# Kernel tuning notes

Hardware: AMD Instinct MI355X
Metric: run time of the kernel (lower is better)

## Reference

```python
import jax, jax.numpy as jnp
import numpy as np

P = 64  # number of parameters per grid cell
# torch.combinations(param, 2, with_replacement=True) enumerates (i,j) with i<=j
# in row-major order, which matches np.triu_indices.
IDX_I, IDX_J = np.triu_indices(P)  # each length C = P*(P+1)//2 = 2080


def setup_inputs() -> dict:
    key = jax.random.key(0)
    k1, k2 = jax.random.split(key)
    # [B, G1, G2, P]
    param_tensor = jax.random.normal(k1, (32, 64, 64, P), dtype=jnp.float32)
    # [G1, G2, C]
    coeffs = jax.random.normal(k2, (64, 64, len(IDX_I)), dtype=jnp.float32)
    return {"param_tensor": param_tensor, "coeffs": coeffs}


def reference(param_tensor, coeffs):
    # Pairwise products with replacement: p_i * p_j for i <= j  -> [B,G1,G2,C]
    pair = param_tensor[..., IDX_I] * param_tensor[..., IDX_J]
    # Per-cell weighted sum over combinations, then sum over the 2D grid -> [B]
    cell = jnp.einsum('bijc,ijc->bij', pair, coeffs)
    return cell.sum(axis=(1, 2))
```

## Files before the change

kernel.cpp:

```cpp
#include <hip/hip_runtime.h>

#define NP     64
#define NC     2080
#define NCELLS 4096
#define NB     32
#define CELLS_PER_BLOCK 4
#define BLOCKS (NCELLS / CELLS_PER_BLOCK)

typedef short bf16x8 __attribute__((ext_vector_type(8)));
typedef float f32x16 __attribute__((ext_vector_type(16)));

__device__ __forceinline__ short f2bf(float f) {
  unsigned u = __float_as_uint(f);
  u += 0x7fffu + ((u >> 16) & 1u);
  return (short)(u >> 16);
}

__global__ __launch_bounds__(256, 4) void poly_mfma_kernel(
    const float* __restrict__ param,
    const float* __restrict__ coeffs,
    float* __restrict__ ws) {
  __shared__ float scoef[CELLS_PER_BLOCK][NC];
  __shared__ float sred[CELLS_PER_BLOCK][NB];

  const int tid  = threadIdx.x;
  const int wave = tid >> 6;
  const int lane = tid & 63;
  const int lo5  = lane & 31;
  const int hi   = lane >> 5;
  const int cell = blockIdx.x * CELLS_PER_BLOCK + wave;

  {
    const float4* gsrc =
        reinterpret_cast<const float4*>(coeffs + (size_t)cell * NC);
    float4* ldst = reinterpret_cast<float4*>(&scoef[wave][0]);
#pragma unroll
    for (int k = 0; k < 8; ++k) ldst[k * 64 + lane] = gsrc[k * 64 + lane];
    if (lane < 8) ldst[512 + lane] = gsrc[512 + lane];
  }

  const float* pb = param + ((size_t)lo5 * NCELLS + cell) * NP;
  bf16x8 afrag[4];
#pragma unroll
  for (int ks = 0; ks < 4; ++ks) {
#pragma unroll
    for (int eh = 0; eh < 2; ++eh) {
      const int i0 = ks * 16 + 4 * hi + 8 * eh;
      const float4 v = *reinterpret_cast<const float4*>(pb + i0);
      afrag[ks][eh * 4 + 0] = f2bf(v.x);
      afrag[ks][eh * 4 + 1] = f2bf(v.y);
      afrag[ks][eh * 4 + 2] = f2bf(v.z);
      afrag[ks][eh * 4 + 3] = f2bf(v.w);
    }
  }

  const float* sw = &scoef[wave][0];
  f32x16 acc0, acc1;
#pragma unroll
  for (int r = 0; r < 16; ++r) { acc0[r] = 0.f; acc1[r] = 0.f; }

#pragma unroll
  for (int ks = 0; ks < 4; ++ks) {
    bf16x8 b0, b1;
#pragma unroll
    for (int e = 0; e < 8; ++e) {
      const int i = ks * 16 + 4 * hi + (e & 3) + 8 * (e >> 2);
      const int cbase = i * (127 - i) / 2;
      const float v0 = (lo5 >= i) ? sw[cbase + lo5] : 0.f;
      const float v1 = (lo5 + 32 >= i) ? sw[cbase + lo5 + 32] : 0.f;
      b0[e] = f2bf(v0);
      b1[e] = f2bf(v1);
    }
    acc0 = __builtin_amdgcn_mfma_f32_32x32x16_bf16(afrag[ks], b0, acc0, 0, 0, 0);
    acc1 = __builtin_amdgcn_mfma_f32_32x32x16_bf16(afrag[ks], b1, acc1, 0, 0, 0);
  }

  float dacc[16];
#pragma unroll
  for (int r = 0; r < 16; ++r) {
    const int b = (r & 3) + 8 * (r >> 2) + 4 * hi;
    const float* pe = param + ((size_t)b * NCELLS + cell) * NP;
    dacc[r] = fmaf(acc0[r], pe[lo5], acc1[r] * pe[lo5 + 32]);
  }

#pragma unroll
  for (int r = 0; r < 16; ++r) {
    float v = dacc[r];
    v += __shfl_xor(v, 1, 64);
    v += __shfl_xor(v, 2, 64);
    v += __shfl_xor(v, 4, 64);
    v += __shfl_xor(v, 8, 64);
    v += __shfl_xor(v, 16, 64);
    dacc[r] = v;
  }
  if (lo5 == 0) {
#pragma unroll
    for (int r = 0; r < 16; ++r) {
      const int b = (r & 3) + 8 * (r >> 2) + 4 * hi;
      sred[wave][b] = dacc[r];
    }
  }
  __syncthreads();
  if (tid < NB) {
    ws[(size_t)blockIdx.x * NB + tid] =
        sred[0][tid] + sred[1][tid] + sred[2][tid] + sred[3][tid];
  }
}

__global__ void poly_reduce_kernel(const float* __restrict__ ws,
                                   float* __restrict__ out) {
  __shared__ float sred[8][NB];
  const int tid = threadIdx.x;
  const int b = tid & 31;
  const int part = tid >> 5;
  float s = 0.f;
  for (int k = 0; k < BLOCKS / 8; ++k) {
    s += ws[(size_t)(part * (BLOCKS / 8) + k) * NB + b];
  }
  sred[part][b] = s;
  __syncthreads();
  if (tid < NB) {
    float t = 0.f;
#pragma unroll
    for (int q = 0; q < 8; ++q) t += sred[q][tid];
    out[tid] = t;
  }
}

extern "C" void kernel_launch(void* const* d_in, const int* in_sizes, int n_in,
                              void* d_out, int out_size, void* d_ws,
                              size_t ws_size, hipStream_t stream) {
  const float* param = (const float*)d_in[0];
  const float* coeffs = (const float*)d_in[1];
  float* out = (float*)d_out;
  float* ws = (float*)d_ws;

  hipLaunchKernelGGL(poly_mfma_kernel, dim3(BLOCKS), dim3(256), 0, stream,
                     param, coeffs, ws);
  hipLaunchKernelGGL(poly_reduce_kernel, dim3(1), dim3(256), 0, stream, ws,
                     out);
}
```

Measured before the change: 24.26 us.

## Store coefficients as bf16 in LDS, prefetch epilogue params, parallelize final reduction

Coefficients are now converted to bf16 once during a block-cooperative load into a half-sized padded LDS buffer, so the MFMA loop reads shorts instead of converting floats each time. The epilogue parameter loads are issued before the MFMA loop to hide their latency. The workspace is transposed so the final reduction runs as 32 blocks, one per batch element, each doing a vectorized load and a shuffle reduction instead of a single block looping serially. A block-wide barrier is added after the LDS fill, and the prefetched values raise register pressure.

```diff
diff --git a/kernel.cpp b/kernel.cpp
--- a/kernel.cpp
+++ b/kernel.cpp
@@ -6,9 +6,11 @@
 #define NB     32
 #define CELLS_PER_BLOCK 4
 #define BLOCKS (NCELLS / CELLS_PER_BLOCK)
+#define CSTRIDE 2112
 
-typedef short bf16x8 __attribute__((ext_vector_type(8)));
-typedef float f32x16 __attribute__((ext_vector_type(16)));
+typedef short bf16x8  __attribute__((ext_vector_type(8)));
+typedef short short4v __attribute__((ext_vector_type(4)));
+typedef float f32x16  __attribute__((ext_vector_type(16)));
 
 __device__ __forceinline__ short f2bf(float f) {
   unsigned u = __float_as_uint(f);
@@ -20,7 +22,7 @@
     const float* __restrict__ param,
     const float* __restrict__ coeffs,
     float* __restrict__ ws) {
-  __shared__ float scoef[CELLS_PER_BLOCK][NC];
+  __shared__ short scoefh[CELLS_PER_BLOCK][CSTRIDE];
   __shared__ float sred[CELLS_PER_BLOCK][NB];
 
   const int tid  = threadIdx.x;
@@ -28,15 +30,25 @@
   const int lane = tid & 63;
   const int lo5  = lane & 31;
   const int hi   = lane >> 5;
-  const int cell = blockIdx.x * CELLS_PER_BLOCK + wave;
+  const int cellbase = blockIdx.x * CELLS_PER_BLOCK;
+  const int cell = cellbase + wave;
 
   {
     const float4* gsrc =
-        reinterpret_cast<const float4*>(coeffs + (size_t)cell * NC);
-    float4* ldst = reinterpret_cast<float4*>(&scoef[wave][0]);
+        reinterpret_cast<const float4*>(coeffs + (size_t)cellbase * NC);
 #pragma unroll
-    for (int k = 0; k < 8; ++k) ldst[k * 64 + lane] = gsrc[k * 64 + lane];
-    if (lane < 8) ldst[512 + lane] = gsrc[512 + lane];
+    for (int k = 0; k < 9; ++k) {
+      const int idx = tid + k * 256;
+      if (idx < (CELLS_PER_BLOCK * NC) / 4) {
+        const int cl = idx / 520;
+        const int q  = idx - cl * 520;
+        const float4 v = gsrc[idx];
+        short4v h;
+        h[0] = f2bf(v.x); h[1] = f2bf(v.y);
+        h[2] = f2bf(v.z); h[3] = f2bf(v.w);
+        *reinterpret_cast<short4v*>(&scoefh[cl][4 * q]) = h;
+      }
+    }
   }
 
   const float* pb = param + ((size_t)lo5 * NCELLS + cell) * NP;
@@ -54,7 +66,18 @@
     }
   }
 
-  const float* sw = &scoef[wave][0];
+  __syncthreads();
+
+  float pepi0[16], pepi1[16];
+#pragma unroll
+  for (int r = 0; r < 16; ++r) {
+    const int b = (r & 3) + 8 * (r >> 2) + 4 * hi;
+    const float* pe = param + ((size_t)b * NCELLS + cell) * NP;
+    pepi0[r] = pe[lo5];
+    pepi1[r] = pe[lo5 + 32];
+  }
+
+  const short* sw = &scoefh[wave][0];
   f32x16 acc0, acc1;
 #pragma unroll
   for (int r = 0; r < 16; ++r) { acc0[r] = 0.f; acc1[r] = 0.f; }
@@ -66,10 +89,10 @@
     for (int e = 0; e < 8; ++e) {
       const int i = ks * 16 + 4 * hi + (e & 3) + 8 * (e >> 2);
       const int cbase = i * (127 - i) / 2;
-      const float v0 = (lo5 >= i) ? sw[cbase + lo5] : 0.f;
-      const float v1 = (lo5 + 32 >= i) ? sw[cbase + lo5 + 32] : 0.f;
-      b0[e] = f2bf(v0);
-      b1[e] = f2bf(v1);
+      const short v0 = sw[cbase + lo5];
+      const short v1 = sw[cbase + lo5 + 32];
+      b0[e] = (lo5 >= i) ? v0 : (short)0;
+      b1[e] = (lo5 + 32 >= i) ? v1 : (short)0;
     }
     acc0 = __builtin_amdgcn_mfma_f32_32x32x16_bf16(afrag[ks], b0, acc0, 0, 0, 0);
     acc1 = __builtin_amdgcn_mfma_f32_32x32x16_bf16(afrag[ks], b1, acc1, 0, 0, 0);
@@ -77,11 +100,8 @@
 
   float dacc[16];
 #pragma unroll
-  for (int r = 0; r < 16; ++r) {
-    const int b = (r & 3) + 8 * (r >> 2) + 4 * hi;
-    const float* pe = param + ((size_t)b * NCELLS + cell) * NP;
-    dacc[r] = fmaf(acc0[r], pe[lo5], acc1[r] * pe[lo5 + 32]);
-  }
+  for (int r = 0; r < 16; ++r)
+    dacc[r] = fmaf(acc0[r], pepi0[r], acc1[r] * pepi1[r]);
 
 #pragma unroll
   for (int r = 0; r < 16; ++r) {
@@ -102,29 +122,24 @@
   }
   __syncthreads();
   if (tid < NB) {
-    ws[(size_t)blockIdx.x * NB + tid] =
+    ws[(size_t)tid * BLOCKS + blockIdx.x] =
         sred[0][tid] + sred[1][tid] + sred[2][tid] + sred[3][tid];
   }
 }
 
 __global__ void poly_reduce_kernel(const float* __restrict__ ws,
                                    float* __restrict__ out) {
-  __shared__ float sred[8][NB];
+  const int b = blockIdx.x;
   const int tid = threadIdx.x;
-  const int b = tid & 31;
-  const int part = tid >> 5;
-  float s = 0.f;
-  for (int k = 0; k < BLOCKS / 8; ++k) {
-    s += ws[(size_t)(part * (BLOCKS / 8) + k) * NB + b];
-  }
-  sred[part][b] = s;
+  const float4 v =
+      reinterpret_cast<const float4*>(ws + (size_t)b * BLOCKS)[tid];
+  float s = (v.x + v.y) + (v.z + v.w);
+#pragma unroll
+  for (int off = 1; off <= 32; off <<= 1) s += __shfl_xor(s, off, 64);
+  __shared__ float sp[4];
+  if ((tid & 63) == 0) sp[tid >> 6] = s;
   __syncthreads();
-  if (tid < NB) {
-    float t = 0.f;
-#pragma unroll
-    for (int q = 0; q < 8; ++q) t += sred[q][tid];
-    out[tid] = t;
-  }
+  if (tid == 0) out[b] = (sp[0] + sp[1]) + (sp[2] + sp[3]);
 }
 
 extern "C" void kernel_launch(void* const* d_in, const int* in_sizes, int n_in,
@@ -137,6 +152,6 @@
 
   hipLaunchKernelGGL(poly_mfma_kernel, dim3(BLOCKS), dim3(256), 0, stream,
                      param, coeffs, ws);
-  hipLaunchKernelGGL(poly_reduce_kernel, dim3(1), dim3(256), 0, stream, ws,
+  hipLaunchKernelGGL(poly_reduce_kernel, dim3(NB), dim3(256), 0, stream, ws,
                      out);
 }
```

Measured after the change: 22.30 us. 1.09x faster.
